# Kernel optimization log

Hardware: AMD Instinct MI355X
Metric: run time of the kernel (lower is better)

Reference implementation:

```python
import jax, jax.numpy as jnp
import numpy as np

NUM_HEADS = 16


def setup_inputs() -> dict:
    key = jax.random.key(0)
    ks = jax.random.split(key, 7)
    B, N, C, P = 8, 1024, 1024, 64
    H, hd = NUM_HEADS, C // NUM_HEADS
    return {
        "x": jax.random.normal(ks[0], (B, N, C), jnp.float32),
        "prompt": jax.random.normal(ks[1], (B, 2, P, H, hd), jnp.float32),
        "alpha": jax.random.uniform(ks[2], (1,), jnp.float32),
        "half_alpha": jax.random.uniform(ks[3], (1,), jnp.float32),
        "Wqkv": jax.random.normal(ks[4], (3 * C, C), jnp.float32) * 0.02,
        "Wproj": jax.random.normal(ks[5], (C, C), jnp.float32) * 0.02,
        "bproj": jnp.zeros((C,), jnp.float32),
    }


def reference(x, prompt, alpha, half_alpha, Wqkv, Wproj, bproj):
    B, N, C = x.shape
    H = NUM_HEADS
    hd = C // H
    scale = hd ** -0.5
    a = alpha[0]
    ha = half_alpha[0]
    # QKV projection (no bias): [B,N,3C] -> [3,B,H,N,hd]
    qkv = (x @ Wqkv.T).reshape(B, N, 3, H, hd).transpose(2, 0, 3, 1, 4)
    q, k, v = qkv[0], qkv[1], qkv[2]
    # prompt [B,2,P,H,hd] -> [2,B,H,P,hd]
    pr = prompt.transpose(1, 0, 3, 2, 4)
    key_prefix, value_prefix = pr[0], pr[1]
    # prefix concat with elementwise scaling
    k = jnp.concatenate([key_prefix, k * ha], axis=2) * a  # [B,H,P+N,hd]
    v = jnp.concatenate([value_prefix, v * ha], axis=2) * a
    attn = jax.nn.softmax(jnp.einsum('bhqd,bhkd->bhqk', q, k) * scale, axis=-1)
    out = jnp.einsum('bhqk,bhkd->bhqd', attn, v)  # [B,H,N,hd]
    out = out.transpose(0, 2, 1, 3).reshape(B, N, C)
    return out @ Wproj.T + bproj
```

## Files before the change

kernel.cpp:

```cpp
#include <hip/hip_runtime.h>

typedef float f32x4 __attribute__((ext_vector_type(4)));
typedef short bf16x8 __attribute__((ext_vector_type(8)));

#define NB 8
#define NH 16
#define NSEQ 1024
#define NP 64
#define NKV 1088
#define NC 1024
#define NHD 64

__device__ __forceinline__ unsigned short f2bf(float f) {
  unsigned int u = __builtin_bit_cast(unsigned int, f);
  u += 0x7fffu + ((u >> 16) & 1u);
  return (unsigned short)(u >> 16);
}

__device__ __forceinline__ void gload16(const void* g, void* l) {
  __builtin_amdgcn_global_load_lds((const __attribute__((address_space(1))) void*)g,
                                   (__attribute__((address_space(3))) void*)l, 16, 0, 0);
}

__device__ __forceinline__ f32x4 mfma16(bf16x8 a, bf16x8 b, f32x4 c) {
  return __builtin_amdgcn_mfma_f32_16x16x32_bf16(a, b, c, 0, 0, 0);
}

__device__ __forceinline__ size_t fa_elem(int r, int k) {
  return (size_t)(r >> 7) * 131072 + (size_t)(k >> 6) * 8192 + ((r >> 6) & 1) * 4096 +
         ((k >> 5) & 1) * 2048 + ((r >> 4) & 3) * 512 + (((k >> 3) & 3) * 16 + (r & 15)) * 8 +
         (k & 7);
}

__device__ __forceinline__ void fragpack_chunk(const float* __restrict__ src,
                                               unsigned short* __restrict__ dst, int c) {
  const int lane = c & 63, m = (c >> 6) & 3, kk = (c >> 8) & 1, wr = (c >> 9) & 1,
            t = (c >> 10) & 15, panel = c >> 14;
  const int row = panel * 128 + wr * 64 + m * 16 + (lane & 15);
  const int k = t * 64 + kk * 32 + (lane >> 4) * 8;
  const float* s = src + (size_t)row * 1024 + k;
  const float4 v0 = *(const float4*)s;
  const float4 v1 = *(const float4*)(s + 4);
  ushort4 o0, o1;
  o0.x = f2bf(v0.x); o0.y = f2bf(v0.y); o0.z = f2bf(v0.z); o0.w = f2bf(v0.w);
  o1.x = f2bf(v1.x); o1.y = f2bf(v1.y); o1.z = f2bf(v1.z); o1.w = f2bf(v1.w);
  *(ushort4*)(dst + (size_t)c * 8) = o0;
  *(ushort4*)(dst + (size_t)c * 8 + 4) = o1;
}

__global__ void pack_fused(const float* __restrict__ x, const float* __restrict__ wq,
                           const float* __restrict__ wp, const float* __restrict__ prompt,
                           unsigned short* __restrict__ xd, unsigned short* __restrict__ wqd,
                           unsigned short* __restrict__ wpd, unsigned short* __restrict__ Kg,
                           unsigned short* __restrict__ Vt, const float* __restrict__ alpha) {
  int gid = blockIdx.x * 256 + threadIdx.x;
  if (gid < 1048576) {
    fragpack_chunk(x, xd, gid);
  } else if (gid < 1441792) {
    fragpack_chunk(wq, wqd, gid - 1048576);
  } else if (gid < 1572864) {
    fragpack_chunk(wp, wpd, gid - 1441792);
  } else {
    int i = gid - 1572864;
    float a = alpha[0];
    int d4 = i & 15, p = (i >> 4) & 63, h = (i >> 10) & 15, b = i >> 14;
    const float4 kv = *(const float4*)(prompt + ((((size_t)(b * 2 + 0) * NP + p) * NH + h) * NHD + d4 * 4));
    ushort4 ko;
    ko.x = f2bf(kv.x * a); ko.y = f2bf(kv.y * a); ko.z = f2bf(kv.z * a); ko.w = f2bf(kv.w * a);
    *(ushort4*)(Kg + (((size_t)(b * NH + h) * NKV + p) * NHD + d4 * 4)) = ko;
    const float4 vv = *(const float4*)(prompt + ((((size_t)(b * 2 + 1) * NP + p) * NH + h) * NHD + d4 * 4));
    size_t vbase = ((size_t)(b * NH + h) * NHD + d4 * 4) * NKV + p;
    Vt[vbase]            = f2bf(vv.x * a);
    Vt[vbase + NKV]      = f2bf(vv.y * a);
    Vt[vbase + 2 * NKV]  = f2bf(vv.z * a);
    Vt[vbase + 3 * NKV]  = f2bf(vv.w * a);
  }
}

template <int MODE>
__global__ __launch_bounds__(256, 2)
void gemm_direct(const unsigned short* __restrict__ Af, const unsigned short* __restrict__ Bf,
                 unsigned short* __restrict__ Qg, unsigned short* __restrict__ Kg,
                 unsigned short* __restrict__ Vt,
                 const float* __restrict__ alphap, const float* __restrict__ halfp,
                 float* __restrict__ Cout, const float* __restrict__ bias) {
  const int tid = threadIdx.x, lane = tid & 63, wv = tid >> 6;
  const int wr = wv >> 1, wc = wv & 1;
  const int lg = lane >> 4, lr = lane & 15;
  const int bx = blockIdx.x, by = blockIdx.y;

  const unsigned short* Ab = Af + (size_t)bx * 131072 + wr * 4096 + lane * 8;
  const unsigned short* Bb = Bf + (size_t)by * 131072 + wc * 4096 + lane * 8;

  f32x4 acc[4][4] = {};
  bf16x8 aC[2][4], bC[2][4], aN[2][4], bN[2][4];

#define LOADA(dst, t)                                                          \
  _Pragma("unroll") for (int kk = 0; kk < 2; ++kk)                             \
  _Pragma("unroll") for (int m = 0; m < 4; ++m)                                \
      dst[kk][m] = *(const bf16x8*)(Ab + (size_t)(t) * 8192 + kk * 2048 + m * 512)
#define LOADB(dst, t)                                                          \
  _Pragma("unroll") for (int kk = 0; kk < 2; ++kk)                             \
  _Pragma("unroll") for (int n = 0; n < 4; ++n)                                \
      dst[kk][n] = *(const bf16x8*)(Bb + (size_t)(t) * 8192 + kk * 2048 + n * 512)

  LOADA(aC, 0);
  LOADB(bC, 0);
#pragma unroll
  for (int t = 0; t < 16; ++t) {
    if (t < 15) { LOADA(aN, t + 1); LOADB(bN, t + 1); }
    __builtin_amdgcn_s_setprio(1);
#pragma unroll
    for (int kk = 0; kk < 2; ++kk)
#pragma unroll
      for (int m = 0; m < 4; ++m)
#pragma unroll
        for (int n = 0; n < 4; ++n)
          acc[m][n] = mfma16(aC[kk][m], bC[kk][n], acc[m][n]);
    __builtin_amdgcn_s_setprio(0);
#pragma unroll
    for (int kk = 0; kk < 2; ++kk)
#pragma unroll
      for (int i = 0; i < 4; ++i) { aC[kk][i] = aN[kk][i]; bC[kk][i] = bN[kk][i]; }
  }
#undef LOADA
#undef LOADB

  if constexpr (MODE == 0) {
    const int slot = (by * 128) >> 10;
    const int csIn = (by * 128) & 1023;
    const float sc = (slot == 0) ? 0.18033688011112042f : (alphap[0] * halfp[0]);
#pragma unroll
    for (int m = 0; m < 4; ++m) {
      const int grow0 = bx * 128 + wr * 64 + m * 16 + lg * 4;
#pragma unroll
      for (int n = 0; n < 4; ++n) {
        const int gcol = csIn + wc * 64 + n * 16 + lr;
        const int h = gcol >> 6, d = gcol & 63;
#pragma unroll
        for (int j = 0; j < 4; ++j) {
          const int grow = grow0 + j;
          const int b = grow >> 10, nn = grow & 1023;
          const unsigned short u = f2bf(acc[m][n][j] * sc);
          if (slot == 0)      Qg[(((size_t)b * NH + h) * NSEQ + nn) * NHD + d] = u;
          else if (slot == 1) Kg[(((size_t)b * NH + h) * NKV + NP + nn) * NHD + d] = u;
          else                Vt[(((size_t)b * NH + h) * NHD + d) * NKV + NP + nn] = u;
        }
      }
    }
  } else {
#pragma unroll
    for (int m = 0; m < 4; ++m) {
      const int grow0 = bx * 128 + wr * 64 + m * 16 + lg * 4;
#pragma unroll
      for (int n = 0; n < 4; ++n) {
        const int gcol = by * 128 + wc * 64 + n * 16 + lr;
        const float bb = bias[gcol];
#pragma unroll
        for (int j = 0; j < 4; ++j)
          Cout[(size_t)(grow0 + j) * NC + gcol] = acc[m][n][j] + bb;
      }
    }
  }
}

__global__ __launch_bounds__(256, 3)
void attn_fwd(const unsigned short* __restrict__ Qg, const unsigned short* __restrict__ Kg,
              const unsigned short* __restrict__ Vt, unsigned short* __restrict__ Oat) {
  __shared__ __align__(16) unsigned short Klds[2][64 * 64];
  __shared__ __align__(16) unsigned short Vlds[2][64 * 64];
  __shared__ __align__(16) unsigned short Plds[4 * 32 * 64];
  const int tid = threadIdx.x, lane = tid & 63, wv = tid >> 6;
  const int bh = blockIdx.x & 127;
  const int q0 = (blockIdx.x >> 7) * 128;
  const int lg = lane >> 4, lr = lane & 15;

  bf16x8 bq[2][2];
#pragma unroll
  for (int nq = 0; nq < 2; ++nq)
#pragma unroll
    for (int kk = 0; kk < 2; ++kk)
      bq[nq][kk] = *(const bf16x8*)(Qg + ((size_t)bh * NSEQ + q0 + wv * 32 + nq * 16 + lr) * NHD + kk * 32 + lg * 8);

  f32x4 oac[2][4] = {};
  float mrun[2] = {-1e30f, -1e30f};
  float lrun[2] = {0.f, 0.f};

  const int kr0 = tid >> 3, kc = tid & 7;
  const int sw = kc ^ (kr0 & 7);
  const unsigned short* Kgp = Kg + ((size_t)bh * NKV + kr0) * NHD + sw * 8;
  const unsigned short* Vgp = Vt + ((size_t)bh * NHD + kr0) * NKV + sw * 8;
  unsigned short* Pw = Plds + wv * 2048;

#define STAGE(t, bsel)                                                      \
  do {                                                                      \
    unsigned short* kb = &Klds[bsel][0] + wv * 512;                         \
    unsigned short* vb = &Vlds[bsel][0] + wv * 512;                         \
    gload16(Kgp + (size_t)(t) * 4096, kb);                                  \
    gload16(Kgp + (size_t)(t) * 4096 + 32 * NHD, kb + 2048);                \
    gload16(Vgp + (size_t)(t) * 64, vb);                                    \
    gload16(Vgp + (size_t)(t) * 64 + (size_t)32 * NKV, vb + 2048);          \
  } while (0)

  STAGE(0, 0);
  asm volatile("s_waitcnt vmcnt(0)" ::: "memory");
  __builtin_amdgcn_s_barrier();

  for (int t = 0; t < 17; ++t) {
    const int b = t & 1;
    if (t < 16) STAGE(t + 1, b ^ 1);

    f32x4 sa[4][2] = {};
    __builtin_amdgcn_s_setprio(1);
#pragma unroll
    for (int kk = 0; kk < 2; ++kk) {
      bf16x8 ak[4];
#pragma unroll
      for (int mk = 0; mk < 4; ++mk) {
        const int row = mk * 16 + lr;
        const int cc = (kk * 4 + lg) ^ (row & 7);
        ak[mk] = *(const bf16x8*)(&Klds[b][0] + row * 64 + cc * 8);
      }
#pragma unroll
      for (int mk = 0; mk < 4; ++mk)
#pragma unroll
        for (int nq = 0; nq < 2; ++nq)
          sa[mk][nq] = mfma16(ak[mk], bq[nq][kk], sa[mk][nq]);
    }
    __builtin_amdgcn_s_setprio(0);

    float tmx[2];
#pragma unroll
    for (int nq = 0; nq < 2; ++nq) {
      f32x4 m4 = sa[0][nq];
#pragma unroll
      for (int mk = 1; mk < 4; ++mk)
#pragma unroll
        for (int j = 0; j < 4; ++j) m4[j] = fmaxf(m4[j], sa[mk][nq][j]);
      float tm = fmaxf(fmaxf(m4[0], m4[1]), fmaxf(m4[2], m4[3]));
      tm = fmaxf(tm, __shfl_xor(tm, 16));
      tm = fmaxf(tm, __shfl_xor(tm, 32));
      tmx[nq] = tm;
    }
    const bool upd = !__all((tmx[0] <= mrun[0] + 8.f) && (tmx[1] <= mrun[1] + 8.f));
    if (upd) {
      const float nm0 = fmaxf(mrun[0], tmx[0]);
      const float nm1 = fmaxf(mrun[1], tmx[1]);
      const float e0 = __builtin_amdgcn_exp2f(mrun[0] - nm0);
      const float e1 = __builtin_amdgcn_exp2f(mrun[1] - nm1);
      mrun[0] = nm0; mrun[1] = nm1;
      lrun[0] *= e0; lrun[1] *= e1;
#pragma unroll
      for (int m = 0; m < 2; ++m)
#pragma unroll
        for (int j = 0; j < 4; ++j) {
          const float fe = __shfl(m ? e1 : e0, lg * 4 + j, 16);
#pragma unroll
          for (int df = 0; df < 4; ++df) oac[m][df][j] *= fe;
        }
    }
#pragma unroll
    for (int nq = 0; nq < 2; ++nq) {
#pragma unroll
      for (int mk = 0; mk < 4; ++mk)
#pragma unroll
        for (int j = 0; j < 4; ++j)
          sa[mk][nq][j] = __builtin_amdgcn_exp2f(sa[mk][nq][j] - mrun[nq]);
      f32x4 s4 = sa[0][nq];
#pragma unroll
      for (int mk = 1; mk < 4; ++mk)
#pragma unroll
        for (int j = 0; j < 4; ++j) s4[j] += sa[mk][nq][j];
      float s = (s4[0] + s4[1]) + (s4[2] + s4[3]);
      s += __shfl_xor(s, 16);
      s += __shfl_xor(s, 32);
      lrun[nq] += s;
      const int q = nq * 16 + lr;
#pragma unroll
      for (int mk = 0; mk < 4; ++mk) {
        const int c = mk * 2 + (lg >> 1);
        uint2 uu;
        uu.x = (unsigned)f2bf(sa[mk][nq][0]) | ((unsigned)f2bf(sa[mk][nq][1]) << 16);
        uu.y = (unsigned)f2bf(sa[mk][nq][2]) | ((unsigned)f2bf(sa[mk][nq][3]) << 16);
        *(uint2*)(Pw + q * 64 + ((c ^ (q & 7)) << 3) + (lg & 1) * 4) = uu;
      }
    }

    __builtin_amdgcn_s_setprio(1);
#pragma unroll
    for (int kk = 0; kk < 2; ++kk) {
      bf16x8 bv[4], ap[2];
#pragma unroll
      for (int df = 0; df < 4; ++df) {
        const int d = df * 16 + lr;
        const int cc = (kk * 4 + lg) ^ (d & 7);
        bv[df] = *(const bf16x8*)(&Vlds[b][0] + d * 64 + cc * 8);
      }
#pragma unroll
      for (int m = 0; m < 2; ++m) {
        const int q = m * 16 + lr;
        const int pos = (kk * 4 + lg) ^ (q & 7);
        ap[m] = *(const bf16x8*)(Pw + q * 64 + pos * 8);
      }
#pragma unroll
      for (int m = 0; m < 2; ++m)
#pragma unroll
        for (int df = 0; df < 4; ++df)
          oac[m][df] = mfma16(ap[m], bv[df], oac[m][df]);
    }
    __builtin_amdgcn_s_setprio(0);

    asm volatile("s_waitcnt vmcnt(0)" ::: "memory");
    __builtin_amdgcn_s_barrier();
  }
#undef STAGE

  const int bidx = bh >> 4, h = bh & 15;
  const float l0 = 1.f / lrun[0], l1 = 1.f / lrun[1];
#pragma unroll
  for (int m = 0; m < 2; ++m) {
#pragma unroll
    for (int j = 0; j < 4; ++j) {
      const float fi = __shfl(m ? l1 : l0, lg * 4 + j, 16);
      const int grow = bidx * NSEQ + q0 + wv * 32 + m * 16 + lg * 4 + j;
#pragma unroll
      for (int df = 0; df < 4; ++df) {
        const int col = h * 64 + df * 16 + lr;
        Oat[fa_elem(grow, col)] = f2bf(oac[m][df][j] * fi);
      }
    }
  }
}

extern "C" void kernel_launch(void* const* d_in, const int* in_sizes, int n_in,
                              void* d_out, int out_size, void* d_ws, size_t ws_size,
                              hipStream_t stream) {
  const float* x      = (const float*)d_in[0];
  const float* prompt = (const float*)d_in[1];
  const float* alpha  = (const float*)d_in[2];
  const float* halfa  = (const float*)d_in[3];
  const float* Wqkv   = (const float*)d_in[4];
  const float* Wproj  = (const float*)d_in[5];
  const float* bproj  = (const float*)d_in[6];
  float* out = (float*)d_out;

  unsigned short* ws    = (unsigned short*)d_ws;
  unsigned short* x_bf  = ws;
  unsigned short* w_bf  = x_bf + (size_t)8192 * 1024;
  unsigned short* wp_bf = w_bf + (size_t)3072 * 1024;
  unsigned short* Qg    = wp_bf + (size_t)1024 * 1024;
  unsigned short* Kg    = Qg + (size_t)NB * NH * NSEQ * NHD;
  unsigned short* Vt    = Kg + (size_t)NB * NH * NKV * NHD;
  unsigned short* Oat   = Vt + (size_t)NB * NH * NKV * NHD;

  pack_fused<<<6656, 256, 0, stream>>>(x, Wqkv, Wproj, prompt, x_bf, w_bf, wp_bf,
                                       Kg, Vt, alpha);

  gemm_direct<0><<<dim3(64, 24), 256, 0, stream>>>(x_bf, w_bf, Qg, Kg, Vt, alpha, halfa,
                                                   nullptr, nullptr);
  attn_fwd<<<1024, 256, 0, stream>>>(Qg, Kg, Vt, Oat);
  gemm_direct<1><<<dim3(64, 8), 256, 0, stream>>>(Oat, wp_bf, nullptr, nullptr, nullptr,
                                                  nullptr, nullptr, out, bproj);
}
```

Measured before the change: 177.0 us.

## Store K/V in MFMA fragment order and load directly from global, dropping LDS staging

The QKV GEMM epilogue and the prompt packing now write K and V into a per-(batch,head) layout that matches the MFMA operand fragment order. The attention kernel then loads K and V fragments straight from global memory into registers, removing the LDS double buffer, the global-to-LDS async loads and the per-tile barriers. A sched_barrier is also added in the GEMM main loop to pin the order of loads and MFMAs. In exchange, every wave independently reads the full K/V stream from global or L2 with no sharing inside the block, and the GEMM epilogue now does scattered 2-byte stores.

```diff
diff --git a/kernel.cpp b/kernel.cpp
--- a/kernel.cpp
+++ b/kernel.cpp
@@ -10,16 +10,12 @@
 #define NKV 1088
 #define NC 1024
 #define NHD 64
+#define BHSZ 69632
 
 __device__ __forceinline__ unsigned short f2bf(float f) {
   unsigned int u = __builtin_bit_cast(unsigned int, f);
   u += 0x7fffu + ((u >> 16) & 1u);
   return (unsigned short)(u >> 16);
-}
-
-__device__ __forceinline__ void gload16(const void* g, void* l) {
-  __builtin_amdgcn_global_load_lds((const __attribute__((address_space(1))) void*)g,
-                                   (__attribute__((address_space(3))) void*)l, 16, 0, 0);
 }
 
 __device__ __forceinline__ f32x4 mfma16(bf16x8 a, bf16x8 b, f32x4 c) {
@@ -51,8 +47,8 @@
 __global__ void pack_fused(const float* __restrict__ x, const float* __restrict__ wq,
                            const float* __restrict__ wp, const float* __restrict__ prompt,
                            unsigned short* __restrict__ xd, unsigned short* __restrict__ wqd,
-                           unsigned short* __restrict__ wpd, unsigned short* __restrict__ Kg,
-                           unsigned short* __restrict__ Vt, const float* __restrict__ alpha) {
+                           unsigned short* __restrict__ wpd, unsigned short* __restrict__ Kf,
+                           unsigned short* __restrict__ Vf, const float* __restrict__ alpha) {
   int gid = blockIdx.x * 256 + threadIdx.x;
   if (gid < 1048576) {
     fragpack_chunk(x, xd, gid);
@@ -64,24 +60,32 @@
     int i = gid - 1572864;
     float a = alpha[0];
     int d4 = i & 15, p = (i >> 4) & 63, h = (i >> 10) & 15, b = i >> 14;
-    const float4 kv = *(const float4*)(prompt + ((((size_t)(b * 2 + 0) * NP + p) * NH + h) * NHD + d4 * 4));
-    ushort4 ko;
-    ko.x = f2bf(kv.x * a); ko.y = f2bf(kv.y * a); ko.z = f2bf(kv.z * a); ko.w = f2bf(kv.w * a);
-    *(ushort4*)(Kg + (((size_t)(b * NH + h) * NKV + p) * NHD + d4 * 4)) = ko;
-    const float4 vv = *(const float4*)(prompt + ((((size_t)(b * 2 + 1) * NP + p) * NH + h) * NHD + d4 * 4));
-    size_t vbase = ((size_t)(b * NH + h) * NHD + d4 * 4) * NKV + p;
-    Vt[vbase]            = f2bf(vv.x * a);
-    Vt[vbase + NKV]      = f2bf(vv.y * a);
-    Vt[vbase + 2 * NKV]  = f2bf(vv.z * a);
-    Vt[vbase + 3 * NKV]  = f2bf(vv.w * a);
+    const int bh = b * 16 + h;
+    const int d0 = d4 * 4;
+    const float4 kv4 = *(const float4*)(prompt + ((((size_t)(b * 2 + 0) * NP + p) * NH + h) * NHD + d0));
+    {
+      const int mk = p >> 4, lrk = p & 15, kk = d0 >> 5, lg = (d0 >> 3) & 3, e0 = d0 & 7;
+      unsigned short* kd = Kf + (size_t)bh * BHSZ + ((mk * 2 + kk) * 4 + lg) * 128 + lrk * 8 + e0;
+      kd[0] = f2bf(kv4.x * a); kd[1] = f2bf(kv4.y * a);
+      kd[2] = f2bf(kv4.z * a); kd[3] = f2bf(kv4.w * a);
+    }
+    const float4 vv4 = *(const float4*)(prompt + ((((size_t)(b * 2 + 1) * NP + p) * NH + h) * NHD + d0));
+    {
+      const int df = d0 >> 4, kk = p >> 5, lg = (p >> 3) & 3, e = p & 7;
+      unsigned short* vd = Vf + (size_t)bh * BHSZ + ((df * 2 + kk) * 4 + lg) * 128 + e;
+      vd[((d0 + 0) & 15) * 8] = f2bf(vv4.x * a);
+      vd[((d0 + 1) & 15) * 8] = f2bf(vv4.y * a);
+      vd[((d0 + 2) & 15) * 8] = f2bf(vv4.z * a);
+      vd[((d0 + 3) & 15) * 8] = f2bf(vv4.w * a);
+    }
   }
 }
 
 template <int MODE>
 __global__ __launch_bounds__(256, 2)
 void gemm_direct(const unsigned short* __restrict__ Af, const unsigned short* __restrict__ Bf,
-                 unsigned short* __restrict__ Qg, unsigned short* __restrict__ Kg,
-                 unsigned short* __restrict__ Vt,
+                 unsigned short* __restrict__ Qg, unsigned short* __restrict__ Kf,
+                 unsigned short* __restrict__ Vf,
                  const float* __restrict__ alphap, const float* __restrict__ halfp,
                  float* __restrict__ Cout, const float* __restrict__ bias) {
   const int tid = threadIdx.x, lane = tid & 63, wv = tid >> 6;
@@ -109,6 +113,7 @@
 #pragma unroll
   for (int t = 0; t < 16; ++t) {
     if (t < 15) { LOADA(aN, t + 1); LOADB(bN, t + 1); }
+    __builtin_amdgcn_sched_barrier(0);
     __builtin_amdgcn_s_setprio(1);
 #pragma unroll
     for (int kk = 0; kk < 2; ++kk)
@@ -141,10 +146,21 @@
         for (int j = 0; j < 4; ++j) {
           const int grow = grow0 + j;
           const int b = grow >> 10, nn = grow & 1023;
+          const int bh = b * 16 + h;
           const unsigned short u = f2bf(acc[m][n][j] * sc);
-          if (slot == 0)      Qg[(((size_t)b * NH + h) * NSEQ + nn) * NHD + d] = u;
-          else if (slot == 1) Kg[(((size_t)b * NH + h) * NKV + NP + nn) * NHD + d] = u;
-          else                Vt[(((size_t)b * NH + h) * NHD + d) * NKV + NP + nn] = u;
+          if (slot == 0) {
+            Qg[((size_t)bh * NSEQ + nn) * NHD + d] = u;
+          } else if (slot == 1) {
+            const int kv = NP + nn;
+            const int t = kv >> 6, mk = (kv >> 4) & 3, lrk = kv & 15;
+            const int kkk = d >> 5, lgk = (d >> 3) & 3, e = d & 7;
+            Kf[(size_t)bh * BHSZ + (size_t)((t * 4 + mk) * 2 + kkk) * 512 + (lgk * 16 + lrk) * 8 + e] = u;
+          } else {
+            const int kv = NP + nn;
+            const int t = kv >> 6, kkv = (kv >> 5) & 1, lgv = (kv >> 3) & 3, e = kv & 7;
+            const int df = d >> 4, lrv = d & 15;
+            Vf[(size_t)bh * BHSZ + (size_t)((t * 4 + df) * 2 + kkv) * 512 + (lgv * 16 + lrv) * 8 + e] = u;
+          }
         }
       }
     }
@@ -165,10 +181,8 @@
 }
 
 __global__ __launch_bounds__(256, 3)
-void attn_fwd(const unsigned short* __restrict__ Qg, const unsigned short* __restrict__ Kg,
-              const unsigned short* __restrict__ Vt, unsigned short* __restrict__ Oat) {
-  __shared__ __align__(16) unsigned short Klds[2][64 * 64];
-  __shared__ __align__(16) unsigned short Vlds[2][64 * 64];
+void attn_fwd(const unsigned short* __restrict__ Qg, const unsigned short* __restrict__ Kf,
+              const unsigned short* __restrict__ Vf, unsigned short* __restrict__ Oat) {
   __shared__ __align__(16) unsigned short Plds[4 * 32 * 64];
   const int tid = threadIdx.x, lane = tid & 63, wv = tid >> 6;
   const int bh = blockIdx.x & 127;
@@ -186,48 +200,35 @@
   float mrun[2] = {-1e30f, -1e30f};
   float lrun[2] = {0.f, 0.f};
 
-  const int kr0 = tid >> 3, kc = tid & 7;
-  const int sw = kc ^ (kr0 & 7);
-  const unsigned short* Kgp = Kg + ((size_t)bh * NKV + kr0) * NHD + sw * 8;
-  const unsigned short* Vgp = Vt + ((size_t)bh * NHD + kr0) * NKV + sw * 8;
+  const unsigned short* Kb = Kf + (size_t)bh * BHSZ + lane * 8;
+  const unsigned short* Vb = Vf + (size_t)bh * BHSZ + lane * 8;
   unsigned short* Pw = Plds + wv * 2048;
 
-#define STAGE(t, bsel)                                                      \
-  do {                                                                      \
-    unsigned short* kb = &Klds[bsel][0] + wv * 512;                         \
-    unsigned short* vb = &Vlds[bsel][0] + wv * 512;                         \
-    gload16(Kgp + (size_t)(t) * 4096, kb);                                  \
-    gload16(Kgp + (size_t)(t) * 4096 + 32 * NHD, kb + 2048);                \
-    gload16(Vgp + (size_t)(t) * 64, vb);                                    \
-    gload16(Vgp + (size_t)(t) * 64 + (size_t)32 * NKV, vb + 2048);          \
-  } while (0)
-
-  STAGE(0, 0);
-  asm volatile("s_waitcnt vmcnt(0)" ::: "memory");
-  __builtin_amdgcn_s_barrier();
-
   for (int t = 0; t < 17; ++t) {
-    const int b = t & 1;
-    if (t < 16) STAGE(t + 1, b ^ 1);
+    bf16x8 ak[4][2];
+#pragma unroll
+    for (int mk = 0; mk < 4; ++mk)
+#pragma unroll
+      for (int kk = 0; kk < 2; ++kk)
+        ak[mk][kk] = *(const bf16x8*)(Kb + (size_t)((t * 4 + mk) * 2 + kk) * 512);
 
     f32x4 sa[4][2] = {};
     __builtin_amdgcn_s_setprio(1);
 #pragma unroll
-    for (int kk = 0; kk < 2; ++kk) {
-      bf16x8 ak[4];
-#pragma unroll
-      for (int mk = 0; mk < 4; ++mk) {
-        const int row = mk * 16 + lr;
-        const int cc = (kk * 4 + lg) ^ (row & 7);
-        ak[mk] = *(const bf16x8*)(&Klds[b][0] + row * 64 + cc * 8);
-      }
+    for (int kk = 0; kk < 2; ++kk)
 #pragma unroll
       for (int mk = 0; mk < 4; ++mk)
 #pragma unroll
         for (int nq = 0; nq < 2; ++nq)
-          sa[mk][nq] = mfma16(ak[mk], bq[nq][kk], sa[mk][nq]);
-    }
+          sa[mk][nq] = mfma16(ak[mk][kk], bq[nq][kk], sa[mk][nq]);
     __builtin_amdgcn_s_setprio(0);
+
+    bf16x8 bv[4][2];
+#pragma unroll
+    for (int df = 0; df < 4; ++df)
+#pragma unroll
+      for (int kk = 0; kk < 2; ++kk)
+        bv[df][kk] = *(const bf16x8*)(Vb + (size_t)((t * 4 + df) * 2 + kk) * 512);
 
     float tmx[2];
 #pragma unroll
@@ -289,13 +290,7 @@
     __builtin_amdgcn_s_setprio(1);
 #pragma unroll
     for (int kk = 0; kk < 2; ++kk) {
-      bf16x8 bv[4], ap[2];
-#pragma unroll
-      for (int df = 0; df < 4; ++df) {
-        const int d = df * 16 + lr;
-        const int cc = (kk * 4 + lg) ^ (d & 7);
-        bv[df] = *(const bf16x8*)(&Vlds[b][0] + d * 64 + cc * 8);
-      }
+      bf16x8 ap[2];
 #pragma unroll
       for (int m = 0; m < 2; ++m) {
         const int q = m * 16 + lr;
@@ -306,14 +301,10 @@
       for (int m = 0; m < 2; ++m)
 #pragma unroll
         for (int df = 0; df < 4; ++df)
-          oac[m][df] = mfma16(ap[m], bv[df], oac[m][df]);
+          oac[m][df] = mfma16(ap[m], bv[df][kk], oac[m][df]);
     }
     __builtin_amdgcn_s_setprio(0);
-
-    asm volatile("s_waitcnt vmcnt(0)" ::: "memory");
-    __builtin_amdgcn_s_barrier();
-  }
-#undef STAGE
+  }
 
   const int bidx = bh >> 4, h = bh & 15;
   const float l0 = 1.f / lrun[0], l1 = 1.f / lrun[1];
@@ -349,16 +340,16 @@
   unsigned short* w_bf  = x_bf + (size_t)8192 * 1024;
   unsigned short* wp_bf = w_bf + (size_t)3072 * 1024;
   unsigned short* Qg    = wp_bf + (size_t)1024 * 1024;
-  unsigned short* Kg    = Qg + (size_t)NB * NH * NSEQ * NHD;
-  unsigned short* Vt    = Kg + (size_t)NB * NH * NKV * NHD;
-  unsigned short* Oat   = Vt + (size_t)NB * NH * NKV * NHD;
+  unsigned short* Kf    = Qg + (size_t)NB * NH * NSEQ * NHD;
+  unsigned short* Vf    = Kf + (size_t)128 * BHSZ;
+  unsigned short* Oat   = Vf + (size_t)128 * BHSZ;
 
   pack_fused<<<6656, 256, 0, stream>>>(x, Wqkv, Wproj, prompt, x_bf, w_bf, wp_bf,
-                                       Kg, Vt, alpha);
-
-  gemm_direct<0><<<dim3(64, 24), 256, 0, stream>>>(x_bf, w_bf, Qg, Kg, Vt, alpha, halfa,
+                                       Kf, Vf, alpha);
+
+  gemm_direct<0><<<dim3(64, 24), 256, 0, stream>>>(x_bf, w_bf, Qg, Kf, Vf, alpha, halfa,
                                                    nullptr, nullptr);
-  attn_fwd<<<1024, 256, 0, stream>>>(Qg, Kg, Vt, Oat);
+  attn_fwd<<<1024, 256, 0, stream>>>(Qg, Kf, Vf, Oat);
   gemm_direct<1><<<dim3(64, 8), 256, 0, stream>>>(Oat, wp_bf, nullptr, nullptr, nullptr,
                                                   nullptr, nullptr, out, bproj);
 }
```

Result: faster. 165.3 us (-6.6%).
